# Optimization experiments

Hardware: AMD Instinct MI355X
Metric: run time of the kernel (lower is better)

Reference implementation:

```python
import jax, jax.numpy as jnp
import numpy as np

B, S, E, H = 2, 2048, 2048, 16
HD = E // H  # head_dim = 128


def _rope(x):
    # x: (B, S, H, HD). Faithful to source: sin/cos built from head_dim,
    # but _rotate_every_two operates on the SEQUENCE axis (axis 1) and the
    # rearrange 'b d j ... -> b (d j) ...' with d=2 concatenates, not interleaves.
    s, hd = x.shape[1], x.shape[-1]
    inv_freq = 1.0 / 10000 ** (np.arange(0, hd, 2) / hd)          # (hd/2,)
    sinusoid = np.einsum('i,j->ij', np.arange(s), inv_freq)       # (s, hd/2)
    # einops.repeat 'b n -> b (n j)', j=2 interleaves each element twice
    sin = np.repeat(np.sin(sinusoid), 2, axis=1)[-s:, None, :]    # (s, 1, hd)
    cos = np.repeat(np.cos(sinusoid), 2, axis=1)[-s:, None, :]
    sin = jnp.asarray(sin, x.dtype)
    cos = jnp.asarray(cos, x.dtype)
    odds = x[:, 1::2]   # (B, S/2, H, HD)
    evens = x[:, ::2]
    rot = jnp.concatenate([-odds, evens], axis=1)  # (B, S, H, HD)
    return x * cos + rot * sin


def setup_inputs() -> dict:
    key = jax.random.key(0)
    k_in, kq, kk, kv, ko = jax.random.split(key, 5)
    scale_in = (1.0 / E) ** 0.5   # lecun_normal fan_in = E
    scale_out = (1.0 / E) ** 0.5  # out_proj fan_in = H*HD = E
    return {
        'inputs': jax.random.normal(k_in, (B, S, E), dtype=jnp.float32),
        'mask': jnp.zeros((1, 1, S, S), dtype=jnp.float32),
        'wq': jax.random.normal(kq, (E, H, HD), dtype=jnp.float32) * scale_in,
        'wk': jax.random.normal(kk, (E, H, HD), dtype=jnp.float32) * scale_in,
        'wv': jax.random.normal(kv, (E, H, HD), dtype=jnp.float32) * scale_in,
        'wo': jax.random.normal(ko, (H, HD, E), dtype=jnp.float32) * scale_out,
        'train': 0,
    }


def reference(inputs, mask, wq, wk, wv, wo, train):
    # QKV projections: (B,S,E) x (E,H,HD) -> (B,S,H,HD)
    q = jnp.einsum('bse,ehd->bshd', inputs, wq)
    k = jnp.einsum('bse,ehd->bshd', inputs, wk)
    v = jnp.einsum('bse,ehd->bshd', inputs, wv)
    q = _rope(q)
    k = _rope(k)
    # scores + custom norm: x / (2*hidden_dim)**(-0.5) == x * sqrt(2*E)
    norm_scale = (2.0 * E) ** 0.5
    qk = jnp.einsum('bshe,bShe->bhsS', q, k)
    attn = jax.nn.softmax((qk + mask) * norm_scale, axis=-1)
    self_attn = jnp.einsum('bhsS,bShe->bshe', attn, v)  # (B,S,H,HD)
    # out projection contracts (heads, kv): (B,S,H,HD) x (H,HD,E) -> (B,S,E)
    return jnp.einsum('bshd,hde->bse', self_attn, wo)
```

## Files before the change

kernel.cpp:

```cpp
#include <hip/hip_runtime.h>
#include <hip/hip_bf16.h>
#include <cmath>

#define Bn 2
#define Sn 2048
#define En 2048
#define Hn 16
#define HDn 128
#define Mn (Bn*Sn)
#define NORMS2 92.33248261689366f

typedef __attribute__((ext_vector_type(8))) short short8;
typedef __attribute__((ext_vector_type(4))) float f32x4;

__device__ __forceinline__ short f2bf(float x) {
    __hip_bfloat16 h = __float2bfloat16(x);
    return *reinterpret_cast<short*>(&h);
}
__device__ __forceinline__ float bf2f(short s) {
    __hip_bfloat16 h = *reinterpret_cast<__hip_bfloat16*>(&s);
    return __bfloat162float(h);
}
__device__ __forceinline__ void gl_lds16(const void* g, void* l) {
    __builtin_amdgcn_global_load_lds(
        (const __attribute__((address_space(1))) unsigned int*)g,
        (__attribute__((address_space(3))) unsigned int*)l, 16, 0, 0);
}

#if __has_builtin(__builtin_amdgcn_exp2f)
#define EXP2(x) __builtin_amdgcn_exp2f(x)
#else
#define EXP2(x) exp2f(x)
#endif

template<int CTRL>
__device__ __forceinline__ float dppf(float x) {
    int r = __builtin_amdgcn_update_dpp(0, __builtin_bit_cast(int, x), CTRL, 0xf, 0xf, true);
    return __builtin_bit_cast(float, r);
}
__device__ __forceinline__ float redmax16(float x) {
    x = fmaxf(x, dppf<0xB1>(x));
    x = fmaxf(x, dppf<0x4E>(x));
    x = fmaxf(x, dppf<0x141>(x));
    x = fmaxf(x, dppf<0x140>(x));
    return x;
}
__device__ __forceinline__ float redsum16(float x) {
    x += dppf<0xB1>(x);
    x += dppf<0x4E>(x);
    x += dppf<0x141>(x);
    x += dppf<0x140>(x);
    return x;
}

static __global__ void rope_table_kernel(float* __restrict__ sinT, float* __restrict__ cosT) {
    int i = blockIdx.x * 256 + threadIdx.x;
    int t = i >> 6, f = i & 63;
    double inv = pow(10000.0, -(double)(2 * f) / (double)HDn);
    double ang = (double)t * inv;
    sinT[i] = (float)sin(ang);
    cosT[i] = (float)cos(ang);
}

static __global__ void split_x_kernel(const float* __restrict__ X,
                                      short* __restrict__ Xhi, short* __restrict__ Xlo) {
    int i = (blockIdx.x * 256 + threadIdx.x) * 4;
    float4 x = *(const float4*)&X[i];
    short4 hi, lo;
    hi.x = f2bf(x.x); lo.x = f2bf(x.x - bf2f(hi.x));
    hi.y = f2bf(x.y); lo.y = f2bf(x.y - bf2f(hi.y));
    hi.z = f2bf(x.z); lo.z = f2bf(x.z - bf2f(hi.z));
    hi.w = f2bf(x.w); lo.w = f2bf(x.w - bf2f(hi.w));
    *(short4*)&Xhi[i] = hi;
    *(short4*)&Xlo[i] = lo;
}

template<bool SPLIT>
static __global__ __launch_bounds__(256) void wtrans_kernel(const float* __restrict__ W,
        short* __restrict__ Thi, short* __restrict__ Tlo) {
    __shared__ float tile[32][33];
    int tx = threadIdx.x & 31, ty = threadIdx.x >> 5;
    int k0 = blockIdx.y * 32, n0 = blockIdx.x * 32;
    #pragma unroll
    for (int i = 0; i < 4; ++i)
        tile[ty + i * 8][tx] = W[(size_t)(k0 + ty + i * 8) * En + n0 + tx];
    __syncthreads();
    #pragma unroll
    for (int i = 0; i < 4; ++i) {
        float v = tile[tx][ty + i * 8];
        size_t idx = (size_t)(n0 + ty + i * 8) * En + k0 + tx;
        short hv = f2bf(v);
        Thi[idx] = hv;
        if (SPLIT) Tlo[idx] = f2bf(v - bf2f(hv));
    }
}

template<int NPROD, int OUTMODE>
static __global__ __launch_bounds__(256) void gemm_kernel(
        const short* __restrict__ Ahi, const short* __restrict__ Alo,
        const short* __restrict__ Bhi, const short* __restrict__ Blo,
        float* __restrict__ Cf, short* __restrict__ Cbt, short* __restrict__ Clo) {
    __shared__ short As_hi[128 * 32];
    __shared__ short Bs_hi[128 * 32];
    __shared__ short As_lo[NPROD == 3 ? 128 * 32 : 8];
    __shared__ short Bs_lo[NPROD == 3 ? 128 * 32 : 8];

    const int tid = threadIdx.x;
    const int w = tid >> 6, l = tid & 63;
    const int quad = l >> 4, l15 = l & 15;
    const int wr = (w >> 1) * 64, wc = (w & 1) * 64;
    const int row0 = blockIdx.y * 128, col0 = blockIdx.x * 128;

    const int off0 = tid * 16;
    const int r_a = off0 >> 6;
    const int kb = (off0 & 63) >> 1;

    f32x4 acc[4][4];
    #pragma unroll
    for (int i = 0; i < 4; ++i)
        #pragma unroll
        for (int j = 0; j < 4; ++j) acc[i][j] = f32x4{0.f, 0.f, 0.f, 0.f};

    for (int k0 = 0; k0 < En; k0 += 32) {
        const short* ap = Ahi + (size_t)(row0 + r_a) * En + k0 + kb;
        const short* bp = Bhi + (size_t)(col0 + r_a) * En + k0 + kb;
        gl_lds16(ap,           &As_hi[off0 / 2]);
        gl_lds16(ap + 64 * En, &As_hi[(off0 + 4096) / 2]);
        gl_lds16(bp,           &Bs_hi[off0 / 2]);
        gl_lds16(bp + 64 * En, &Bs_hi[(off0 + 4096) / 2]);
        if constexpr (NPROD == 3) {
            const short* ap2 = Alo + (size_t)(row0 + r_a) * En + k0 + kb;
            const short* bp2 = Blo + (size_t)(col0 + r_a) * En + k0 + kb;
            gl_lds16(ap2,           &As_lo[off0 / 2]);
            gl_lds16(ap2 + 64 * En, &As_lo[(off0 + 4096) / 2]);
            gl_lds16(bp2,           &Bs_lo[off0 / 2]);
            gl_lds16(bp2 + 64 * En, &Bs_lo[(off0 + 4096) / 2]);
        }
        __syncthreads();

        short8 bhf[4], blf[4];
        #pragma unroll
        for (int ni = 0; ni < 4; ++ni) {
            bhf[ni] = *(const short8*)&Bs_hi[(wc + ni * 16 + l15) * 32 + quad * 8];
            if constexpr (NPROD == 3)
                blf[ni] = *(const short8*)&Bs_lo[(wc + ni * 16 + l15) * 32 + quad * 8];
        }
        #pragma unroll
        for (int mi = 0; mi < 4; ++mi) {
            short8 ahf = *(const short8*)&As_hi[(wr + mi * 16 + l15) * 32 + quad * 8];
            short8 alf;
            if constexpr (NPROD == 3)
                alf = *(const short8*)&As_lo[(wr + mi * 16 + l15) * 32 + quad * 8];
            #pragma unroll
            for (int ni = 0; ni < 4; ++ni) {
                acc[mi][ni] = __builtin_amdgcn_mfma_f32_16x16x32_bf16(ahf, bhf[ni], acc[mi][ni], 0, 0, 0);
                if constexpr (NPROD == 3) {
                    acc[mi][ni] = __builtin_amdgcn_mfma_f32_16x16x32_bf16(ahf, blf[ni], acc[mi][ni], 0, 0, 0);
                    acc[mi][ni] = __builtin_amdgcn_mfma_f32_16x16x32_bf16(alf, bhf[ni], acc[mi][ni], 0, 0, 0);
                }
            }
        }
        __syncthreads();
    }

    if constexpr (OUTMODE == 0) {
        #pragma unroll
        for (int mi = 0; mi < 4; ++mi)
            #pragma unroll
            for (int ni = 0; ni < 4; ++ni) {
                int r = row0 + wr + mi * 16 + quad * 4;
                int c = col0 + wc + ni * 16 + l15;
                #pragma unroll
                for (int reg = 0; reg < 4; ++reg)
                    Cf[(size_t)(r + reg) * En + c] = acc[mi][ni][reg];
            }
    } else if constexpr (OUTMODE == 1) {
        #pragma unroll
        for (int mi = 0; mi < 4; ++mi)
            #pragma unroll
            for (int ni = 0; ni < 4; ++ni) {
                int srow = row0 + wr + mi * 16 + quad * 4;
                int c = col0 + wc + ni * 16 + l15;
                int b = srow >> 11, s = srow & (Sn - 1);
                int h = c >> 7, d = c & 127;
                short4 v;
                v.x = f2bf(acc[mi][ni][0]); v.y = f2bf(acc[mi][ni][1]);
                v.z = f2bf(acc[mi][ni][2]); v.w = f2bf(acc[mi][ni][3]);
                *(short4*)&Cbt[((size_t)(b * Hn + h) * HDn + d) * Sn + s] = v;
            }
    } else {
        #pragma unroll
        for (int mi = 0; mi < 4; ++mi)
            #pragma unroll
            for (int ni = 0; ni < 4; ++ni) {
                int r = row0 + wr + mi * 16 + quad * 4;
                int c = col0 + wc + ni * 16 + l15;
                #pragma unroll
                for (int reg = 0; reg < 4; ++reg) {
                    float v = acc[mi][ni][reg];
                    short h = f2bf(v);
                    Cbt[(size_t)(r + reg) * En + c] = h;
                    Clo[(size_t)(r + reg) * En + c] = f2bf(v - bf2f(h));
                }
            }
    }
}

static __global__ void rope_split2_kernel(
        const short* __restrict__ QXh, const short* __restrict__ QXl,
        short* __restrict__ QYh, short* __restrict__ QYl,
        const short* __restrict__ KXh, const short* __restrict__ KXl,
        short* __restrict__ KYh, short* __restrict__ KYl,
        const float* __restrict__ sinT, const float* __restrict__ cosT) {
    int p = blockIdx.x * 256 + threadIdx.x;
    int sel = p >> 22;
    p &= (1 << 22) - 1;
    const short* Xh = sel ? KXh : QXh;
    const short* Xl = sel ? KXl : QXl;
    short* Yh = sel ? KYh : QYh;
    short* Yl = sel ? KYl : QYl;
    int c2 = p & (En / 2 - 1);
    int t = (p >> 10) & (Sn - 1);
    int bb = p >> 21;
    int f = c2 & 63;
    float sv = sinT[(t << 6) + f], cv = cosT[(t << 6) + f];
    int tsrc; float sgn;
    if (t < Sn / 2) { tsrc = 2 * t + 1; sgn = -1.f; }
    else            { tsrc = 2 * (t - Sn / 2); sgn = 1.f; }
    size_t rowt = ((size_t)bb * Sn + t) * En + 2 * c2;
    size_t rows = ((size_t)bb * Sn + tsrc) * En + 2 * c2;
    short2 xh = *(const short2*)&Xh[rowt], xl = *(const short2*)&Xl[rowt];
    short2 sh = *(const short2*)&Xh[rows], sl = *(const short2*)&Xl[rows];
    float x0 = bf2f(xh.x) + bf2f(xl.x), x1 = bf2f(xh.y) + bf2f(xl.y);
    float s0 = bf2f(sh.x) + bf2f(sl.x), s1 = bf2f(sh.y) + bf2f(sl.y);
    float y0 = x0 * cv + sgn * s0 * sv;
    float y1 = x1 * cv + sgn * s1 * sv;
    short2 hi, lo;
    hi.x = f2bf(y0); lo.x = f2bf(y0 - bf2f(hi.x));
    hi.y = f2bf(y1); lo.y = f2bf(y1 - bf2f(hi.y));
    *(short2*)&Yh[rowt] = hi;
    *(short2*)&Yl[rowt] = lo;
}

static __global__ __launch_bounds__(512, 4) void flash4_kernel(
        const short* __restrict__ Qhi, const short* __restrict__ Qlo,
        const short* __restrict__ Khi, const short* __restrict__ Klo,
        const short* __restrict__ Vt, const float* __restrict__ mask,
        short* __restrict__ AO) {
    __shared__ short lds0[34816];

    const int tid = threadIdx.x;
    const int w = tid >> 6, l = tid & 63;
    const int quad = l >> 4, l15 = l & 15;
    const int n = blockIdx.x;
    const int bh = (n & 7) * 4 + ((n >> 3) & 3);
    const int qt = n >> 5;
    const int b = bh >> 4, h = bh & 15;
    const int r0 = qt * 128;
    const size_t qkbase = (size_t)b * Sn * En + (size_t)h * HDn;
    const int psb = 24576 + w * 1280;

    #pragma unroll
    for (int c = 0; c < 4; ++c) {
        int off = tid * 16 + c * 8192;
        int row = off >> 8;
        int gp = (off >> 4) & 15;
        int gl = gp ^ (row & 7);
        size_t gidx = qkbase + (size_t)(r0 + row) * En + gl * 8;
        gl_lds16(Qhi + gidx, &lds0[off / 2]);
        gl_lds16(Qlo + gidx, &lds0[16384 + off / 2]);
    }
    __syncthreads();
    short8 qh[4], ql[4];
    {
        int row = 16 * w + l15;
        #pragma unroll
        for (int kc = 0; kc < 4; ++kc) {
            int gp = (kc * 4 + quad) ^ (row & 7);
            qh[kc] = *(const short8*)&lds0[row * 128 + gp * 8];
            ql[kc] = *(const short8*)&lds0[16384 + row * 128 + gp * 8];
        }
    }

    f32x4 O[8];
    #pragma unroll
    for (int di = 0; di < 8; ++di) O[di] = f32x4{0.f, 0.f, 0.f, 0.f};
    float m_prev[4] = {-INFINITY, -INFINITY, -INFINITY, -INFINITY};
    float l_run[4] = {0.f, 0.f, 0.f, 0.f};
    const int qrow_base = r0 + 16 * w + quad * 4;

    for (int j0 = 0; j0 < Sn; j0 += 64) {
        __syncthreads();
        #pragma unroll
        for (int c = 0; c < 2; ++c) {
            int off = tid * 16 + c * 8192;
            int row = off >> 8;
            int gp = (off >> 4) & 15;
            int gl = gp ^ (row & 7);
            size_t gidx = qkbase + (size_t)(j0 + row) * En + gl * 8;
            gl_lds16(Khi + gidx, &lds0[off / 2]);
            gl_lds16(Klo + gidx, &lds0[8192 + off / 2]);
        }
        #pragma unroll
        for (int c = 0; c < 2; ++c) {
            int off = tid * 16 + c * 8192;
            int vrow = off >> 7;
            int vgp = (off >> 4) & 7;
            int vgl = vgp ^ (vrow & 7);
            size_t vidx = ((size_t)bh * HDn + vrow) * Sn + j0 + vgl * 8;
            gl_lds16(Vt + vidx, &lds0[16384 + off / 2]);
        }
        float mv[4][4];
        #pragma unroll
        for (int ni = 0; ni < 4; ++ni)
            #pragma unroll
            for (int reg = 0; reg < 4; ++reg)
                mv[ni][reg] = mask[(size_t)(qrow_base + reg) * Sn + j0 + ni * 16 + l15];
        __syncthreads();

        f32x4 p[4];
        #pragma unroll
        for (int ni = 0; ni < 4; ++ni) p[ni] = f32x4{0.f, 0.f, 0.f, 0.f};
        #pragma unroll
        for (int ni = 0; ni < 4; ++ni) {
            int col = ni * 16 + l15;
            #pragma unroll
            for (int kc = 0; kc < 4; ++kc) {
                int gp = (kc * 4 + quad) ^ (col & 7);
                short8 kh = *(const short8*)&lds0[col * 128 + gp * 8];
                short8 kl = *(const short8*)&lds0[8192 + col * 128 + gp * 8];
                p[ni] = __builtin_amdgcn_mfma_f32_16x16x32_bf16(qh[kc], kh, p[ni], 0, 0, 0);
                p[ni] = __builtin_amdgcn_mfma_f32_16x16x32_bf16(qh[kc], kl, p[ni], 0, 0, 0);
                p[ni] = __builtin_amdgcn_mfma_f32_16x16x32_bf16(ql[kc], kh, p[ni], 0, 0, 0);
            }
        }

        float rm[4] = {-INFINITY, -INFINITY, -INFINITY, -INFINITY};
        #pragma unroll
        for (int ni = 0; ni < 4; ++ni)
            #pragma unroll
            for (int reg = 0; reg < 4; ++reg) {
                float v = (p[ni][reg] + mv[ni][reg]) * NORMS2;
                p[ni][reg] = v;
                rm[reg] = fmaxf(rm[reg], v);
            }
        #pragma unroll
        for (int reg = 0; reg < 4; ++reg) rm[reg] = redmax16(rm[reg]);
        float al[4], mn[4], rs[4];
        #pragma unroll
        for (int reg = 0; reg < 4; ++reg) {
            mn[reg] = fmaxf(m_prev[reg], rm[reg]);
            al[reg] = EXP2(m_prev[reg] - mn[reg]);
            rs[reg] = 0.f;
        }
        #pragma unroll
        for (int ni = 0; ni < 4; ++ni)
            #pragma unroll
            for (int reg = 0; reg < 4; ++reg) {
                float pe = EXP2(p[ni][reg] - mn[reg]);
                rs[reg] += pe;
                lds0[psb + (quad * 4 + reg) * 80 + ((ni ^ quad) << 4) + l15] = f2bf(pe);
            }
        #pragma unroll
        for (int reg = 0; reg < 4; ++reg) rs[reg] = redsum16(rs[reg]);
        #pragma unroll
        for (int reg = 0; reg < 4; ++reg) {
            l_run[reg] = l_run[reg] * al[reg] + rs[reg];
            m_prev[reg] = mn[reg];
        }
        #pragma unroll
        for (int di = 0; di < 8; ++di)
            #pragma unroll
            for (int reg = 0; reg < 4; ++reg)
                O[di][reg] *= al[reg];

        short8 pa[2];
        #pragma unroll
        for (int kc2 = 0; kc2 < 2; ++kc2) {
            int g = kc2 * 2 + (quad >> 1);
            int gs = g ^ (l15 >> 2);
            pa[kc2] = *(const short8*)&lds0[psb + l15 * 80 + (gs << 4) + (quad & 1) * 8];
        }

        #pragma unroll
        for (int di = 0; di < 8; ++di) {
            int d = di * 16 + l15;
            #pragma unroll
            for (int kc2 = 0; kc2 < 2; ++kc2) {
                int gp = (kc2 * 4 + quad) ^ (d & 7);
                short8 vb = *(const short8*)&lds0[16384 + d * 64 + gp * 8];
                O[di] = __builtin_amdgcn_mfma_f32_16x16x32_bf16(pa[kc2], vb, O[di], 0, 0, 0);
            }
        }
    }

    float inv[4];
    #pragma unroll
    for (int reg = 0; reg < 4; ++reg) inv[reg] = 1.0f / l_run[reg];
    #pragma unroll
    for (int di = 0; di < 8; ++di)
        #pragma unroll
        for (int reg = 0; reg < 4; ++reg) {
            size_t idx = ((size_t)b * Sn + qrow_base + reg) * En + h * HDn + di * 16 + l15;
            AO[idx] = f2bf(O[di][reg] * inv[reg]);
        }
}

extern "C" void kernel_launch(void* const* d_in, const int* in_sizes, int n_in,
                              void* d_out, int out_size, void* d_ws, size_t ws_size,
                              hipStream_t stream) {
    const float* inputs = (const float*)d_in[0];
    const float* mask   = (const float*)d_in[1];
    const float* wq     = (const float*)d_in[2];
    const float* wk     = (const float*)d_in[3];
    const float* wv     = (const float*)d_in[4];
    const float* wo     = (const float*)d_in[5];
    float* out = (float*)d_out;
    (void)in_sizes; (void)n_in; (void)out_size; (void)ws_size;

    char* W8 = (char*)d_ws;
    float* sinT = (float*)(W8 + 0);
    float* cosT = (float*)(W8 + 524288);
    short* Xhi  = (short*)(W8 + 1048576);
    short* Xlo  = (short*)(W8 + 17825792);
    short* WqTh = (short*)(W8 + 34603008);
    short* WqTl = (short*)(W8 + 42991616);
    short* WkTh = (short*)(W8 + 51380224);
    short* WkTl = (short*)(W8 + 59768832);
    short* WvT  = (short*)(W8 + 68157440);
    short* WoT  = (short*)(W8 + 76546048);
    short* Qpre_hi = (short*)(W8 + 84934656);
    short* Qpre_lo = (short*)(W8 + 101711872);
    short* Kpre_hi = (short*)(W8 + 118489088);
    short* Kpre_lo = (short*)(W8 + 135266304);
    short* Qhi = WqTh;
    short* Qlo = WkTh;
    short* Khi = (short*)(W8 + 152043520);
    short* Klo = (short*)(W8 + 168820736);
    short* Vt  = Kpre_hi;
    short* AO  = Xhi;

    rope_table_kernel<<<512, 256, 0, stream>>>(sinT, cosT);
    split_x_kernel<<<8192, 256, 0, stream>>>(inputs, Xhi, Xlo);
    dim3 tg(64, 64);
    wtrans_kernel<true ><<<tg, 256, 0, stream>>>(wq, WqTh, WqTl);
    wtrans_kernel<true ><<<tg, 256, 0, stream>>>(wk, WkTh, WkTl);
    wtrans_kernel<false><<<tg, 256, 0, stream>>>(wv, WvT, nullptr);
    wtrans_kernel<false><<<tg, 256, 0, stream>>>(wo, WoT, nullptr);

    dim3 gg(En / 128, Mn / 128);
    gemm_kernel<3, 2><<<gg, 256, 0, stream>>>(Xhi, Xlo, WqTh, WqTl, nullptr, Qpre_hi, Qpre_lo);
    gemm_kernel<3, 2><<<gg, 256, 0, stream>>>(Xhi, Xlo, WkTh, WkTl, nullptr, Kpre_hi, Kpre_lo);
    rope_split2_kernel<<<32768, 256, 0, stream>>>(Qpre_hi, Qpre_lo, Qhi, Qlo,
                                                  Kpre_hi, Kpre_lo, Khi, Klo, sinT, cosT);
    gemm_kernel<1, 1><<<gg, 256, 0, stream>>>(Xhi, nullptr, WvT, nullptr, nullptr, Vt, nullptr);

    flash4_kernel<<<512, 512, 0, stream>>>(Qhi, Qlo, Khi, Klo, Vt, mask, AO);

    gemm_kernel<1, 0><<<gg, 256, 0, stream>>>(AO, nullptr, WoT, nullptr, out, nullptr, nullptr);
}
```

Before: 766.6 us.

## Fuse Q/K projection GEMMs, pack pre-RoPE output, coalesce V transpose, bf16 pre-scaled mask

```diff
diff --git a/kernel.cpp b/kernel.cpp
--- a/kernel.cpp
+++ b/kernel.cpp
@@ -75,10 +75,26 @@
     *(short4*)&Xlo[i] = lo;
 }
 
-template<bool SPLIT>
-static __global__ __launch_bounds__(256) void wtrans_kernel(const float* __restrict__ W,
-        short* __restrict__ Thi, short* __restrict__ Tlo) {
+static __global__ void maskconv_kernel(const float* __restrict__ M, short* __restrict__ MB) {
+    int i = (blockIdx.x * 256 + threadIdx.x) * 4;
+    float4 m = *(const float4*)&M[i];
+    short4 o;
+    o.x = f2bf(m.x * NORMS2); o.y = f2bf(m.y * NORMS2);
+    o.z = f2bf(m.z * NORMS2); o.w = f2bf(m.w * NORMS2);
+    *(short4*)&MB[i] = o;
+}
+
+static __global__ __launch_bounds__(256) void wtrans4_kernel(
+        const float* __restrict__ Wq, const float* __restrict__ Wk,
+        const float* __restrict__ Wv, const float* __restrict__ Wo,
+        short* __restrict__ QKh, short* __restrict__ QKl,
+        short* __restrict__ VT, short* __restrict__ OT) {
     __shared__ float tile[32][33];
+    const int z = blockIdx.z;
+    const float* W = (z == 0) ? Wq : (z == 1) ? Wk : (z == 2) ? Wv : Wo;
+    short* Th = (z <= 1) ? QKh : (z == 2) ? VT : OT;
+    const int rowoff = (z == 1) ? 2048 : 0;
+    const bool split = (z <= 1);
     int tx = threadIdx.x & 31, ty = threadIdx.x >> 5;
     int k0 = blockIdx.y * 32, n0 = blockIdx.x * 32;
     #pragma unroll
@@ -88,10 +104,10 @@
     #pragma unroll
     for (int i = 0; i < 4; ++i) {
         float v = tile[tx][ty + i * 8];
-        size_t idx = (size_t)(n0 + ty + i * 8) * En + k0 + tx;
+        size_t idx = (size_t)(rowoff + n0 + ty + i * 8) * En + k0 + tx;
         short hv = f2bf(v);
-        Thi[idx] = hv;
-        if (SPLIT) Tlo[idx] = f2bf(v - bf2f(hv));
+        Th[idx] = hv;
+        if (split) QKl[idx] = f2bf(v - bf2f(hv));
     }
 }
 
@@ -99,11 +115,13 @@
 static __global__ __launch_bounds__(256) void gemm_kernel(
         const short* __restrict__ Ahi, const short* __restrict__ Alo,
         const short* __restrict__ Bhi, const short* __restrict__ Blo,
-        float* __restrict__ Cf, short* __restrict__ Cbt, short* __restrict__ Clo) {
+        float* __restrict__ Cf, short* __restrict__ Cbt,
+        int* __restrict__ Qpk, int* __restrict__ Kpk) {
     __shared__ short As_hi[128 * 32];
     __shared__ short Bs_hi[128 * 32];
     __shared__ short As_lo[NPROD == 3 ? 128 * 32 : 8];
     __shared__ short Bs_lo[NPROD == 3 ? 128 * 32 : 8];
+    __shared__ short Ts[OUTMODE == 1 ? 128 * 136 : 8];
 
     const int tid = threadIdx.x;
     const int w = tid >> 6, l = tid & 63;
@@ -179,73 +197,82 @@
         for (int mi = 0; mi < 4; ++mi)
             #pragma unroll
             for (int ni = 0; ni < 4; ++ni) {
-                int srow = row0 + wr + mi * 16 + quad * 4;
-                int c = col0 + wc + ni * 16 + l15;
-                int b = srow >> 11, s = srow & (Sn - 1);
-                int h = c >> 7, d = c & 127;
-                short4 v;
-                v.x = f2bf(acc[mi][ni][0]); v.y = f2bf(acc[mi][ni][1]);
-                v.z = f2bf(acc[mi][ni][2]); v.w = f2bf(acc[mi][ni][3]);
-                *(short4*)&Cbt[((size_t)(b * Hn + h) * HDn + d) * Sn + s] = v;
-            }
+                int dl = wc + ni * 16 + l15;
+                int sl = wr + mi * 16 + quad * 4;
+                #pragma unroll
+                for (int reg = 0; reg < 4; ++reg)
+                    Ts[dl * 136 + sl + reg] = f2bf(acc[mi][ni][reg]);
+            }
+        __syncthreads();
+        int dl = tid >> 1, s0 = (tid & 1) * 64;
+        int b = row0 >> 11, h = col0 >> 7;
+        size_t gbase = ((size_t)(b * Hn + h) * HDn + dl) * Sn + (row0 & (Sn - 1)) + s0;
+        #pragma unroll
+        for (int k = 0; k < 8; ++k) {
+            short8 vv = *(const short8*)&Ts[dl * 136 + s0 + k * 8];
+            *(short8*)&Cbt[gbase + k * 8] = vv;
+        }
     } else {
+        int* dst = (col0 >= 2048) ? Kpk : Qpk;
+        const int cb = col0 & 2047;
         #pragma unroll
         for (int mi = 0; mi < 4; ++mi)
             #pragma unroll
             for (int ni = 0; ni < 4; ++ni) {
                 int r = row0 + wr + mi * 16 + quad * 4;
-                int c = col0 + wc + ni * 16 + l15;
+                int c = cb + wc + ni * 16 + l15;
                 #pragma unroll
                 for (int reg = 0; reg < 4; ++reg) {
                     float v = acc[mi][ni][reg];
-                    short h = f2bf(v);
-                    Cbt[(size_t)(r + reg) * En + c] = h;
-                    Clo[(size_t)(r + reg) * En + c] = f2bf(v - bf2f(h));
+                    short hh = f2bf(v);
+                    short ll = f2bf(v - bf2f(hh));
+                    dst[(size_t)(r + reg) * 2048 + c] =
+                        ((int)(unsigned short)hh << 16) | (unsigned short)ll;
                 }
             }
     }
 }
 
-static __global__ void rope_split2_kernel(
-        const short* __restrict__ QXh, const short* __restrict__ QXl,
-        short* __restrict__ QYh, short* __restrict__ QYl,
-        const short* __restrict__ KXh, const short* __restrict__ KXl,
-        short* __restrict__ KYh, short* __restrict__ KYl,
+static __global__ void rope_pk_kernel(const int* __restrict__ Pre,
+        short* __restrict__ Yh, short* __restrict__ Yl,
         const float* __restrict__ sinT, const float* __restrict__ cosT) {
     int p = blockIdx.x * 256 + threadIdx.x;
-    int sel = p >> 22;
-    p &= (1 << 22) - 1;
-    const short* Xh = sel ? KXh : QXh;
-    const short* Xl = sel ? KXl : QXl;
-    short* Yh = sel ? KYh : QYh;
-    short* Yl = sel ? KYl : QYl;
-    int c2 = p & (En / 2 - 1);
-    int t = (p >> 10) & (Sn - 1);
-    int bb = p >> 21;
-    int f = c2 & 63;
-    float sv = sinT[(t << 6) + f], cv = cosT[(t << 6) + f];
+    int u = p & 511;
+    int t = (p >> 9) & (Sn - 1);
+    int b = p >> 20;
     int tsrc; float sgn;
     if (t < Sn / 2) { tsrc = 2 * t + 1; sgn = -1.f; }
     else            { tsrc = 2 * (t - Sn / 2); sgn = 1.f; }
-    size_t rowt = ((size_t)bb * Sn + t) * En + 2 * c2;
-    size_t rows = ((size_t)bb * Sn + tsrc) * En + 2 * c2;
-    short2 xh = *(const short2*)&Xh[rowt], xl = *(const short2*)&Xl[rowt];
-    short2 sh = *(const short2*)&Xh[rows], sl = *(const short2*)&Xl[rows];
-    float x0 = bf2f(xh.x) + bf2f(xl.x), x1 = bf2f(xh.y) + bf2f(xl.y);
-    float s0 = bf2f(sh.x) + bf2f(sl.x), s1 = bf2f(sh.y) + bf2f(sl.y);
-    float y0 = x0 * cv + sgn * s0 * sv;
-    float y1 = x1 * cv + sgn * s1 * sv;
-    short2 hi, lo;
+    int f0 = (2 * u) & 63, f1 = (2 * u + 1) & 63;
+    float sv0 = sinT[(t << 6) + f0], cv0 = cosT[(t << 6) + f0];
+    float sv1 = sinT[(t << 6) + f1], cv1 = cosT[(t << 6) + f1];
+    size_t rt = ((size_t)(b * Sn + t)) * 512 + u;
+    size_t rs = ((size_t)(b * Sn + tsrc)) * 512 + u;
+    int4 xt = ((const int4*)Pre)[rt];
+    int4 xs = ((const int4*)Pre)[rs];
+    auto up = [](int v) -> float {
+        return bf2f((short)(v >> 16)) + bf2f((short)(v & 0xffff));
+    };
+    float x0 = up(xt.x), x1 = up(xt.y), x2 = up(xt.z), x3 = up(xt.w);
+    float s0 = up(xs.x), s1 = up(xs.y), s2 = up(xs.z), s3 = up(xs.w);
+    float y0 = x0 * cv0 + sgn * s0 * sv0;
+    float y1 = x1 * cv0 + sgn * s1 * sv0;
+    float y2 = x2 * cv1 + sgn * s2 * sv1;
+    float y3 = x3 * cv1 + sgn * s3 * sv1;
+    short4 hi, lo;
     hi.x = f2bf(y0); lo.x = f2bf(y0 - bf2f(hi.x));
     hi.y = f2bf(y1); lo.y = f2bf(y1 - bf2f(hi.y));
-    *(short2*)&Yh[rowt] = hi;
-    *(short2*)&Yl[rowt] = lo;
-}
-
-static __global__ __launch_bounds__(512, 4) void flash4_kernel(
+    hi.z = f2bf(y2); lo.z = f2bf(y2 - bf2f(hi.z));
+    hi.w = f2bf(y3); lo.w = f2bf(y3 - bf2f(hi.w));
+    size_t o = ((size_t)(b * Sn + t)) * En + 4 * u;
+    *(short4*)&Yh[o] = hi;
+    *(short4*)&Yl[o] = lo;
+}
+
+static __global__ __launch_bounds__(512, 2) void flash5_kernel(
         const short* __restrict__ Qhi, const short* __restrict__ Qlo,
         const short* __restrict__ Khi, const short* __restrict__ Klo,
-        const short* __restrict__ Vt, const float* __restrict__ mask,
+        const short* __restrict__ Vt, const short* __restrict__ maskB,
         short* __restrict__ AO) {
     __shared__ short lds0[34816];
 
@@ -315,7 +342,7 @@
         for (int ni = 0; ni < 4; ++ni)
             #pragma unroll
             for (int reg = 0; reg < 4; ++reg)
-                mv[ni][reg] = mask[(size_t)(qrow_base + reg) * Sn + j0 + ni * 16 + l15];
+                mv[ni][reg] = bf2f(maskB[(size_t)(qrow_base + reg) * Sn + j0 + ni * 16 + l15]);
         __syncthreads();
 
         f32x4 p[4];
@@ -340,7 +367,7 @@
         for (int ni = 0; ni < 4; ++ni)
             #pragma unroll
             for (int reg = 0; reg < 4; ++reg) {
-                float v = (p[ni][reg] + mv[ni][reg]) * NORMS2;
+                float v = fmaf(p[ni][reg], NORMS2, mv[ni][reg]);
                 p[ni][reg] = v;
                 rm[reg] = fmaxf(rm[reg], v);
             }
@@ -419,43 +446,39 @@
     (void)in_sizes; (void)n_in; (void)out_size; (void)ws_size;
 
     char* W8 = (char*)d_ws;
-    float* sinT = (float*)(W8 + 0);
-    float* cosT = (float*)(W8 + 524288);
-    short* Xhi  = (short*)(W8 + 1048576);
-    short* Xlo  = (short*)(W8 + 17825792);
-    short* WqTh = (short*)(W8 + 34603008);
-    short* WqTl = (short*)(W8 + 42991616);
-    short* WkTh = (short*)(W8 + 51380224);
-    short* WkTl = (short*)(W8 + 59768832);
-    short* WvT  = (short*)(W8 + 68157440);
-    short* WoT  = (short*)(W8 + 76546048);
-    short* Qpre_hi = (short*)(W8 + 84934656);
-    short* Qpre_lo = (short*)(W8 + 101711872);
-    short* Kpre_hi = (short*)(W8 + 118489088);
-    short* Kpre_lo = (short*)(W8 + 135266304);
-    short* Qhi = WqTh;
-    short* Qlo = WkTh;
-    short* Khi = (short*)(W8 + 152043520);
-    short* Klo = (short*)(W8 + 168820736);
-    short* Vt  = Kpre_hi;
+    float* sinT  = (float*)(W8 + 0);
+    float* cosT  = (float*)(W8 + 524288);
+    short* Xhi   = (short*)(W8 + 1048576);
+    short* Xlo   = (short*)(W8 + 17825792);
+    short* maskB = (short*)(W8 + 34603008);
+    short* WqkTh = (short*)(W8 + 42991616);
+    short* WqkTl = (short*)(W8 + 59768832);
+    short* WvT   = (short*)(W8 + 76546048);
+    short* WoT   = (short*)(W8 + 84934656);
+    int*   Qpk   = (int*)(W8 + 93323264);
+    int*   Kpk   = (int*)(W8 + 126877696);
+    short* Qhi = WqkTh;
+    short* Qlo = WqkTl;
+    short* Khi = (short*)(W8 + 93323264);
+    short* Klo = (short*)(W8 + 110100480);
+    short* Vt  = (short*)(W8 + 126877696);
     short* AO  = Xhi;
 
     rope_table_kernel<<<512, 256, 0, stream>>>(sinT, cosT);
     split_x_kernel<<<8192, 256, 0, stream>>>(inputs, Xhi, Xlo);
-    dim3 tg(64, 64);
-    wtrans_kernel<true ><<<tg, 256, 0, stream>>>(wq, WqTh, WqTl);
-    wtrans_kernel<true ><<<tg, 256, 0, stream>>>(wk, WkTh, WkTl);
-    wtrans_kernel<false><<<tg, 256, 0, stream>>>(wv, WvT, nullptr);
-    wtrans_kernel<false><<<tg, 256, 0, stream>>>(wo, WoT, nullptr);
-
-    dim3 gg(En / 128, Mn / 128);
-    gemm_kernel<3, 2><<<gg, 256, 0, stream>>>(Xhi, Xlo, WqTh, WqTl, nullptr, Qpre_hi, Qpre_lo);
-    gemm_kernel<3, 2><<<gg, 256, 0, stream>>>(Xhi, Xlo, WkTh, WkTl, nullptr, Kpre_hi, Kpre_lo);
-    rope_split2_kernel<<<32768, 256, 0, stream>>>(Qpre_hi, Qpre_lo, Qhi, Qlo,
-                                                  Kpre_hi, Kpre_lo, Khi, Klo, sinT, cosT);
-    gemm_kernel<1, 1><<<gg, 256, 0, stream>>>(Xhi, nullptr, WvT, nullptr, nullptr, Vt, nullptr);
-
-    flash4_kernel<<<512, 512, 0, stream>>>(Qhi, Qlo, Khi, Klo, Vt, mask, AO);
-
-    gemm_kernel<1, 0><<<gg, 256, 0, stream>>>(AO, nullptr, WoT, nullptr, out, nullptr, nullptr);
-}
+    maskconv_kernel<<<4096, 256, 0, stream>>>(mask, maskB);
+    wtrans4_kernel<<<dim3(64, 64, 4), 256, 0, stream>>>(wq, wk, wv, wo,
+                                                        WqkTh, WqkTl, WvT, WoT);
+
+    gemm_kernel<3, 3><<<dim3(32, 32), 256, 0, stream>>>(
+        Xhi, Xlo, WqkTh, WqkTl, nullptr, nullptr, Qpk, Kpk);
+    rope_pk_kernel<<<8192, 256, 0, stream>>>(Qpk, Qhi, Qlo, sinT, cosT);
+    rope_pk_kernel<<<8192, 256, 0, stream>>>(Kpk, Khi, Klo, sinT, cosT);
+    gemm_kernel<1, 1><<<dim3(16, 32), 256, 0, stream>>>(
+        Xhi, nullptr, WvT, nullptr, nullptr, Vt, nullptr, nullptr);
+
+    flash5_kernel<<<512, 512, 0, stream>>>(Qhi, Qlo, Khi, Klo, Vt, maskB, AO);
+
+    gemm_kernel<1, 0><<<dim3(16, 32), 256, 0, stream>>>(
+        AO, nullptr, WoT, nullptr, out, nullptr, nullptr, nullptr);
+}
```

Result: faster. 683.9 us (-10.8%).
